# Performance work log

Measured on AMD Instinct MI355X. Metric: run time of the kernel, lower is better.

Reference implementation:

```python
import jax, jax.numpy as jnp
import numpy as np

B, T, F_IN, H, OUT = 64, 2048, 128, 256, 10
K, STRIDE, C = 5, 2, 64
TC = (T - K) // STRIDE + 1  # 1022


def setup_inputs() -> dict:
    key = jax.random.key(0)
    ks = jax.random.split(key, 10)
    u = lambda k, shape, bound: jax.random.uniform(k, shape, jnp.float32, -bound, bound)
    cb = 1.0 / np.sqrt(F_IN * K)   # torch Conv1d init bound
    lb = 1.0 / np.sqrt(H)          # torch LSTMCell / Linear init bound
    return {
        "input": jax.random.normal(ks[0], (B, T, F_IN), jnp.float32),
        "r": jnp.zeros((TC, B, C), jnp.float32),
        "conv_w": u(ks[1], (C, F_IN, K), cb),
        "conv_b": u(ks[2], (C,), cb),
        "w_ih": u(ks[3], (4 * H, C), lb),
        "w_hh": u(ks[4], (4 * H, H), lb),
        "b_ih": u(ks[5], (4 * H,), lb),
        "b_hh": u(ks[6], (4 * H,), lb),
        "lin_w": u(ks[7], (OUT, H), lb),
        "lin_b": u(ks[8], (OUT,), lb),
        "batch_size": B,
    }


def reference(input, r, conv_w, conv_b, w_ih, w_hh, b_ih, b_hh, lin_w, lin_b, batch_size):
    # F.normalize default: L2 over dim=1 (the time axis here), eps=1e-12
    norm = jnp.sqrt(jnp.sum(input * input, axis=1, keepdims=True))
    x = input / jnp.maximum(norm, 1e-12)
    # Conv1d over time: [B,T,F] -> [B,F,T] -> [B,64,Tc]
    x = jnp.transpose(x, (0, 2, 1))
    y = jax.lax.conv_general_dilated(
        x, conv_w, window_strides=(STRIDE,), padding='VALID',
        dimension_numbers=('NCH', 'OIH', 'NCH')) + conv_b[None, :, None]
    lstm_in = jax.nn.relu(jnp.transpose(y, (2, 0, 1)))  # [Tc, B, 64]

    hdim = w_hh.shape[1]
    bsz = lstm_in.shape[1]

    def step(carry, xt):
        h, c = carry
        gates = xt @ w_ih.T + h @ w_hh.T + b_ih + b_hh
        i, f, g, o = jnp.split(gates, 4, axis=-1)  # torch gate order i,f,g,o
        c = jax.nn.sigmoid(f) * c + jax.nn.sigmoid(i) * jnp.tanh(g)
        h = jax.nn.sigmoid(o) * jnp.tanh(c)
        return (h, c), None

    init = (jnp.zeros((bsz, hdim), lstm_in.dtype), jnp.zeros((bsz, hdim), lstm_in.dtype))
    (h_t, _), _ = jax.lax.scan(step, init, lstm_in)
    return h_t @ lin_w.T + lin_b
```

## Files before the change

### kernel.cpp

```cpp
#include <hip/hip_runtime.h>
#include <stdint.h>

#define B_ 64
#define T_ 2048
#define F_ 128
#define H_ 256
#define TC_ 1022

typedef __bf16 bf16x8 __attribute__((ext_vector_type(8)));
typedef float f32x4 __attribute__((ext_vector_type(4)));
typedef uint u32x4 __attribute__((ext_vector_type(4)));
typedef unsigned long long u64;

__device__ __forceinline__ ushort f2bf(float f) {
    uint32_t u = __builtin_bit_cast(uint32_t, f);
    u += 0x7FFFu + ((u >> 16) & 1u);
    return (ushort)(u >> 16);
}
__device__ __forceinline__ float sigmoidf_(float x) {
    return __builtin_amdgcn_rcpf(1.f + __expf(-x));
}
__device__ __forceinline__ float tanhf_(float x) {
    x = fminf(15.f, fmaxf(-15.f, x));
    float e = __expf(2.f * x);
    return 1.f - 2.f * __builtin_amdgcn_rcpf(e + 1.f);
}

__global__ __launch_bounds__(128) void k_sqsum(const float* __restrict__ in,
                                               float* __restrict__ sq) {
    int b = blockIdx.x >> 4, tq = blockIdx.x & 15, f = threadIdx.x;
    const float* p = in + ((size_t)b * T_ + (size_t)tq * 128) * F_ + f;
    float acc = 0.f;
#pragma unroll 8
    for (int t = 0; t < 128; ++t) { float v = p[(size_t)t * F_]; acc += v * v; }
    atomicAdd(&sq[b * F_ + f], acc);
}

__global__ __launch_bounds__(256) void k_prep(const float* __restrict__ wih, const float* __restrict__ whh,
                                              const float* __restrict__ bih, const float* __restrict__ bhh,
                                              ushort* __restrict__ wbf, float* __restrict__ bias) {
    int e = blockIdx.x * 256 + threadIdx.x;
    if (e < 64 * 16 * 320) {
        int g = e / 5120, m = (e / 320) & 15, k = e % 320;
        int j = (m & 3) * 256 + g * 4 + (m >> 2);
        float v = (k < 64) ? wih[j * 64 + k] : whh[j * 256 + (k - 64)];
        wbf[e] = f2bf(v);
    }
    if (e < 1024) bias[e] = bih[e] + bhh[e];
}

__global__ __launch_bounds__(256) void k_conv(const float* __restrict__ in, const float* __restrict__ cw,
                                              const float* __restrict__ cb, const float* __restrict__ sq,
                                              ushort* __restrict__ li) {
    __shared__ float rn[128];
    __shared__ __align__(16) float xs[67 * 129];
    __shared__ __align__(16) float wl[80 * 68];
    int b = blockIdx.x >> 5, tile = blockIdx.x & 31;
    int tc0 = tile * 32;
    int tid = threadIdx.x;
    if (tid < 128) { float ss = sq[b * 128 + tid]; rn[tid] = 1.f / fmaxf(sqrtf(ss), 1e-12f); }
    __syncthreads();
    const float* ip = in + ((size_t)b * T_ + (size_t)(2 * tc0)) * F_;
    for (int i = tid; i < 67 * 128; i += 256) {
        int r = i >> 7, f = i & 127;
        int t = 2 * tc0 + r;
        xs[r * 129 + f] = (t < T_) ? ip[(size_t)r * F_ + f] * rn[f] : 0.f;
    }
    int cg = tid & 15, tcg = tid >> 4;
    float a00 = 0, a01 = 0, a10 = 0, a11 = 0, a20 = 0, a21 = 0, a30 = 0, a31 = 0;
    for (int fc = 0; fc < 8; ++fc) {
        __syncthreads();
        for (int i = tid; i < 64 * 80; i += 256) {
            int c = i / 80, j = i - c * 80;
            wl[j * 68 + c] = cw[c * 640 + fc * 80 + j];
        }
        __syncthreads();
#pragma unroll
        for (int fi = 0; fi < 16; ++fi) {
#pragma unroll
            for (int k = 0; k < 5; ++k) {
                const float4 w4 = *(const float4*)&wl[(fi * 5 + k) * 68 + cg * 4];
                float x0 = xs[(4 * tcg + k) * 129 + fc * 16 + fi];
                float x1 = xs[(4 * tcg + 2 + k) * 129 + fc * 16 + fi];
                a00 += w4.x * x0; a01 += w4.x * x1;
                a10 += w4.y * x0; a11 += w4.y * x1;
                a20 += w4.z * x0; a21 += w4.z * x1;
                a30 += w4.w * x0; a31 += w4.w * x1;
            }
        }
    }
    float bc0 = cb[cg * 4 + 0], bc1 = cb[cg * 4 + 1], bc2 = cb[cg * 4 + 2], bc3 = cb[cg * 4 + 3];
#pragma unroll
    for (int tt = 0; tt < 2; ++tt) {
        int tc = tc0 + tcg * 2 + tt;
        if (tc < TC_) {
            float v0 = fmaxf((tt ? a01 : a00) + bc0, 0.f);
            float v1 = fmaxf((tt ? a11 : a10) + bc1, 0.f);
            float v2 = fmaxf((tt ? a21 : a20) + bc2, 0.f);
            float v3 = fmaxf((tt ? a31 : a30) + bc3, 0.f);
            uint2 pk;
            pk.x = (uint32_t)f2bf(v0) | ((uint32_t)f2bf(v1) << 16);
            pk.y = (uint32_t)f2bf(v2) | ((uint32_t)f2bf(v3) << 16);
            *reinterpret_cast<uint2*>(&li[((size_t)tc * 64 + b) * 72 + cg * 4]) = pk;
        }
    }
}

__global__ __launch_bounds__(512) void k_scan(const ushort* __restrict__ li,
                                              const ushort* __restrict__ wbf,
                                              const float* __restrict__ bias,
                                              u64* __restrict__ hbuf,
                                              float* __restrict__ hfin) {
    __shared__ __align__(16) ushort Hs[2][16 * 264];
    int p = blockIdx.x & 7, q = blockIdx.x >> 3;
    if (p >= 4) return;
    int tid = threadIdx.x;
    int lane = tid & 63, wave = tid >> 6, l16 = lane & 15, quad = lane >> 4;
    int bb = p * 16 + l16;
    int g2a = q * 16 + 2 * wave, g2b = g2a + 1;
    int u0 = g2a * 4 + quad, u1 = g2b * 4 + quad;
    int pc = 32 * q + 4 * wave + (quad >> 1);
    bf16x8 af0[10], af1[10];
    const ushort* wp0 = wbf + ((size_t)(g2a * 16 + l16)) * 320 + quad * 8;
    const ushort* wp1 = wbf + ((size_t)(g2b * 16 + l16)) * 320 + quad * 8;
#pragma unroll
    for (int s = 0; s < 10; ++s) { af0[s] = *(const bf16x8*)(wp0 + s * 32);
                                   af1[s] = *(const bf16x8*)(wp1 + s * 32); }
    float bi0 = bias[u0], bf0 = bias[256 + u0], bg0 = bias[512 + u0], bo0 = bias[768 + u0];
    float bi1 = bias[u1], bf1 = bias[256 + u1], bg1 = bias[512 + u1], bo1 = bias[768 + u1];
    float cs0 = 0.f, cs1 = 0.f;
    bool broken = false;
    const ushort* xpp = li + ((size_t)0 * 64 + bb) * 72 + quad * 8;
    bf16x8 x0 = *(const bf16x8*)xpp;
    bf16x8 x1 = *(const bf16x8*)(xpp + 32);
#pragma unroll 1
    for (int t = 0; t < TC_; ++t) {
        f32x4 A0 = {0.f, 0.f, 0.f, 0.f}, A1 = {0.f, 0.f, 0.f, 0.f};
        A0 = __builtin_amdgcn_mfma_f32_16x16x32_bf16(af0[0], x0, A0, 0, 0, 0);
        A1 = __builtin_amdgcn_mfma_f32_16x16x32_bf16(af1[0], x0, A1, 0, 0, 0);
        A0 = __builtin_amdgcn_mfma_f32_16x16x32_bf16(af0[1], x1, A0, 0, 0, 0);
        A1 = __builtin_amdgcn_mfma_f32_16x16x32_bf16(af1[1], x1, A1, 0, 0, 0);
        char* hb = (char*)Hs + (size_t)(t & 1) * (16 * 264 * 2);
        if (t > 0) {
            uint tg = (uint)(t - 1);
            const u64* src = hbuf + ((size_t)((t - 1) & 1) << 13) + p * 2048 + tid * 4;
            u64 vv0, vv1, vv2, vv3;
            bool got = false;
            if (!broken) {
                u32x4 pa, pb;
                bool ok;
                int guard = 0;
                do {
                    asm volatile(
                        "global_load_dwordx4 %0, %2, off sc0\n\t"
                        "global_load_dwordx4 %1, %2, off offset:16 sc0\n\t"
                        "s_waitcnt vmcnt(0)"
                        : "=&v"(pa), "=&v"(pb)
                        : "v"(src)
                        : "memory");
                    uint m = ((pa.x >> 16) ^ tg) | ((pa.y >> 16) ^ tg)
                           | ((pa.z >> 16) ^ tg) | ((pa.w >> 16) ^ tg)
                           | ((pb.x >> 16) ^ tg) | ((pb.y >> 16) ^ tg)
                           | ((pb.z >> 16) ^ tg) | ((pb.w >> 16) ^ tg);
                    ok = (m == 0);
                } while (!__all(ok) && ++guard < 1024);
                got = __all(ok);
                if (got) {
                    vv0 = ((u64)pa.y << 32) | pa.x;
                    vv1 = ((u64)pa.w << 32) | pa.z;
                    vv2 = ((u64)pb.y << 32) | pb.x;
                    vv3 = ((u64)pb.w << 32) | pb.z;
                } else {
                    broken = true;
                }
            }
            if (!got) {
                u64 w0, w1, w2, w3;
                bool ok;
                int guard = 0;
                do {
                    w0 = __hip_atomic_load(src + 0, __ATOMIC_RELAXED, __HIP_MEMORY_SCOPE_AGENT);
                    w1 = __hip_atomic_load(src + 1, __ATOMIC_RELAXED, __HIP_MEMORY_SCOPE_AGENT);
                    w2 = __hip_atomic_load(src + 2, __ATOMIC_RELAXED, __HIP_MEMORY_SCOPE_AGENT);
                    w3 = __hip_atomic_load(src + 3, __ATOMIC_RELAXED, __HIP_MEMORY_SCOPE_AGENT);
                    uint m = (((uint)(w0 >> 16) & 0xFFFFu) ^ tg) | (((uint)(w0 >> 48)) ^ tg);
                    m |= (((uint)(w1 >> 16) & 0xFFFFu) ^ tg) | (((uint)(w1 >> 48)) ^ tg);
                    m |= (((uint)(w2 >> 16) & 0xFFFFu) ^ tg) | (((uint)(w2 >> 48)) ^ tg);
                    m |= (((uint)(w3 >> 16) & 0xFFFFu) ^ tg) | (((uint)(w3 >> 48)) ^ tg);
                    ok = (m == 0);
                } while (!__all(ok) && ++guard < (1 << 14));
                vv0 = w0; vv1 = w1; vv2 = w2; vv3 = w3;
            }
            {
                int b = tid >> 5, c0 = (tid * 4) & 127;
                uint4 w;
                w.x = ((uint)vv0 & 0xFFFFu) | (((uint)(vv0 >> 32) & 0xFFFFu) << 16);
                w.y = ((uint)vv1 & 0xFFFFu) | (((uint)(vv1 >> 32) & 0xFFFFu) << 16);
                w.z = ((uint)vv2 & 0xFFFFu) | (((uint)(vv2 >> 32) & 0xFFFFu) << 16);
                w.w = ((uint)vv3 & 0xFFFFu) | (((uint)(vv3 >> 32) & 0xFFFFu) << 16);
                *(uint4*)(hb + b * 528 + c0 * 4) = w;
            }
            __syncthreads();
#pragma unroll
            for (int s = 0; s < 8; ++s) {
                bf16x8 bh = *(const bf16x8*)(hb + l16 * 528 + s * 64 + quad * 16);
                A0 = __builtin_amdgcn_mfma_f32_16x16x32_bf16(af0[2 + s], bh, A0, 0, 0, 0);
                A1 = __builtin_amdgcn_mfma_f32_16x16x32_bf16(af1[2 + s], bh, A1, 0, 0, 0);
            }
        }
        float hv0, hv1;
        {
            float gi = A0[0] + bi0, gf = A0[1] + bf0, gg = A0[2] + bg0, go = A0[3] + bo0;
            float ii = sigmoidf_(gi), ff = sigmoidf_(gf), g2 = tanhf_(gg), oo = sigmoidf_(go);
            cs0 = ff * cs0 + ii * g2;
            hv0 = oo * tanhf_(cs0);
        }
        {
            float gi = A1[0] + bi1, gf = A1[1] + bf1, gg = A1[2] + bg1, go = A1[3] + bo1;
            float ii = sigmoidf_(gi), ff = sigmoidf_(gf), g2 = tanhf_(gg), oo = sigmoidf_(go);
            cs1 = ff * cs1 + ii * g2;
            hv1 = oo * tanhf_(cs1);
        }
        if (t == TC_ - 1) {
            hfin[u0 * 64 + bb] = hv0;
            hfin[u1 * 64 + bb] = hv1;
        } else {
            ushort h0 = f2bf(hv0), h1 = f2bf(hv1);
            uint pr0 = ((uint)h0 & 0xFFFFu) | ((uint)__shfl((int)h0, (lane + 16) & 63) << 16);
            uint pr1 = ((uint)h1 & 0xFFFFu) | ((uint)__shfl((int)h1, (lane + 16) & 63) << 16);
            if ((quad & 1) == 0) {
                uint tg2 = ((uint)t) << 16;
                u64 w0 = (u64)((pr0 & 0xFFFFu) | tg2) | ((u64)((pr0 >> 16) | tg2) << 32);
                u64 w1 = (u64)((pr1 & 0xFFFFu) | tg2) | ((u64)((pr1 >> 16) | tg2) << 32);
                u64* dst = hbuf + ((size_t)(t & 1) << 13) + p * 2048 + l16 * 128;
                __hip_atomic_store(dst + pc, w0, __ATOMIC_RELAXED, __HIP_MEMORY_SCOPE_AGENT);
                __hip_atomic_store(dst + pc + 2, w1, __ATOMIC_RELAXED, __HIP_MEMORY_SCOPE_AGENT);
            }
        }
        int tn = (t + 1 < TC_) ? t + 1 : t;
        const ushort* xpn = li + ((size_t)tn * 64 + bb) * 72 + quad * 8;
        x0 = *(const bf16x8*)xpn;
        x1 = *(const bf16x8*)(xpn + 32);
    }
}

__global__ __launch_bounds__(64) void k_fin(const float* __restrict__ hfin, const float* __restrict__ lw,
                                            const float* __restrict__ lb, float* __restrict__ out) {
    int o = blockIdx.x, b = threadIdx.x;
    float acc = lb[o];
    const float* wp = lw + o * 256;
#pragma unroll 4
    for (int u2 = 0; u2 < 256; ++u2) acc += hfin[u2 * 64 + b] * wp[u2];
    out[b * 10 + o] = acc;
}

extern "C" void kernel_launch(void* const* d_in, const int* in_sizes, int n_in,
                              void* d_out, int out_size, void* d_ws, size_t ws_size,
                              hipStream_t stream) {
    const float* in  = (const float*)d_in[0];
    const float* cw  = (const float*)d_in[2];
    const float* cb  = (const float*)d_in[3];
    const float* wih = (const float*)d_in[4];
    const float* whh = (const float*)d_in[5];
    const float* bih = (const float*)d_in[6];
    const float* bhh = (const float*)d_in[7];
    const float* lw  = (const float*)d_in[8];
    const float* lb  = (const float*)d_in[9];
    float* out = (float*)d_out;

    char* ws = (char*)d_ws;
    float*  sq   = (float*)(ws + 0);
    u64*    hbuf = (u64*)(ws + 32768);
    float*  bias = (float*)(ws + 163840);
    float*  hfin = (float*)(ws + 167936);
    ushort* wbf  = (ushort*)(ws + 233472);
    ushort* li   = (ushort*)(ws + 888832);

    hipMemsetAsync(sq, 0, 32768, stream);
    hipMemsetAsync(hbuf, 0xFF, 131072, stream);

    k_sqsum<<<1024, 128, 0, stream>>>(in, sq);
    k_prep<<<1280, 256, 0, stream>>>(wih, whh, bih, bhh, wbf, bias);
    k_conv<<<2048, 256, 0, stream>>>(in, cw, cb, sq, li);
    k_scan<<<32, 512, 0, stream>>>(li, wbf, bias, hbuf, hfin);
    k_fin<<<10, 64, 0, stream>>>(hfin, lw, lb, out);
}
```

Baseline: 2.547 ms.

## Repartition LSTM scan into fewer, larger 1024-thread blocks

The recurrent scan kernel now runs 16 blocks of 1024 threads, so 8 blocks are active instead of 16. Each active block covers half of the hidden units rather than a quarter, so each batch group exchanges hidden state across 2 blocks instead of 4. Each thread now polls and copies half as much of the shared hidden-state buffer per step. The aim is to cut the cost of the cross-block flag polling on every timestep. In exchange, twice as many waves share each CU's matrix units and the block-wide barrier has more waves to wait for.

```diff
diff --git a/kernel.cpp b/kernel.cpp
--- a/kernel.cpp
+++ b/kernel.cpp
@@ -106,20 +106,20 @@
     }
 }
 
-__global__ __launch_bounds__(512) void k_scan(const ushort* __restrict__ li,
-                                              const ushort* __restrict__ wbf,
-                                              const float* __restrict__ bias,
-                                              u64* __restrict__ hbuf,
-                                              float* __restrict__ hfin) {
+__global__ __launch_bounds__(1024) void k_scan(const ushort* __restrict__ li,
+                                               const ushort* __restrict__ wbf,
+                                               const float* __restrict__ bias,
+                                               u64* __restrict__ hbuf,
+                                               float* __restrict__ hfin) {
     __shared__ __align__(16) ushort Hs[2][16 * 264];
     int p = blockIdx.x & 7, q = blockIdx.x >> 3;
     if (p >= 4) return;
     int tid = threadIdx.x;
     int lane = tid & 63, wave = tid >> 6, l16 = lane & 15, quad = lane >> 4;
     int bb = p * 16 + l16;
-    int g2a = q * 16 + 2 * wave, g2b = g2a + 1;
+    int g2a = q * 32 + wave * 2, g2b = g2a + 1;
     int u0 = g2a * 4 + quad, u1 = g2b * 4 + quad;
-    int pc = 32 * q + 4 * wave + (quad >> 1);
+    int pc = 2 * g2a + (quad >> 1);
     bf16x8 af0[10], af1[10];
     const ushort* wp0 = wbf + ((size_t)(g2a * 16 + l16)) * 320 + quad * 8;
     const ushort* wp1 = wbf + ((size_t)(g2b * 16 + l16)) * 320 + quad * 8;
@@ -143,62 +143,47 @@
         char* hb = (char*)Hs + (size_t)(t & 1) * (16 * 264 * 2);
         if (t > 0) {
             uint tg = (uint)(t - 1);
-            const u64* src = hbuf + ((size_t)((t - 1) & 1) << 13) + p * 2048 + tid * 4;
-            u64 vv0, vv1, vv2, vv3;
+            const u64* src = hbuf + ((size_t)((t - 1) & 1) << 13) + p * 2048 + tid * 2;
+            u64 vv0, vv1;
             bool got = false;
             if (!broken) {
-                u32x4 pa, pb;
+                u32x4 pa;
                 bool ok;
                 int guard = 0;
                 do {
                     asm volatile(
-                        "global_load_dwordx4 %0, %2, off sc0\n\t"
-                        "global_load_dwordx4 %1, %2, off offset:16 sc0\n\t"
+                        "global_load_dwordx4 %0, %1, off sc0\n\t"
                         "s_waitcnt vmcnt(0)"
-                        : "=&v"(pa), "=&v"(pb)
-                        : "v"(src)
-                        : "memory");
+                        : "=&v"(pa) : "v"(src) : "memory");
                     uint m = ((pa.x >> 16) ^ tg) | ((pa.y >> 16) ^ tg)
-                           | ((pa.z >> 16) ^ tg) | ((pa.w >> 16) ^ tg)
-                           | ((pb.x >> 16) ^ tg) | ((pb.y >> 16) ^ tg)
-                           | ((pb.z >> 16) ^ tg) | ((pb.w >> 16) ^ tg);
+                           | ((pa.z >> 16) ^ tg) | ((pa.w >> 16) ^ tg);
                     ok = (m == 0);
                 } while (!__all(ok) && ++guard < 1024);
                 got = __all(ok);
                 if (got) {
                     vv0 = ((u64)pa.y << 32) | pa.x;
                     vv1 = ((u64)pa.w << 32) | pa.z;
-                    vv2 = ((u64)pb.y << 32) | pb.x;
-                    vv3 = ((u64)pb.w << 32) | pb.z;
-                } else {
-                    broken = true;
-                }
+                } else broken = true;
             }
             if (!got) {
-                u64 w0, w1, w2, w3;
+                u64 w0, w1;
                 bool ok;
                 int guard = 0;
                 do {
                     w0 = __hip_atomic_load(src + 0, __ATOMIC_RELAXED, __HIP_MEMORY_SCOPE_AGENT);
                     w1 = __hip_atomic_load(src + 1, __ATOMIC_RELAXED, __HIP_MEMORY_SCOPE_AGENT);
-                    w2 = __hip_atomic_load(src + 2, __ATOMIC_RELAXED, __HIP_MEMORY_SCOPE_AGENT);
-                    w3 = __hip_atomic_load(src + 3, __ATOMIC_RELAXED, __HIP_MEMORY_SCOPE_AGENT);
                     uint m = (((uint)(w0 >> 16) & 0xFFFFu) ^ tg) | (((uint)(w0 >> 48)) ^ tg);
                     m |= (((uint)(w1 >> 16) & 0xFFFFu) ^ tg) | (((uint)(w1 >> 48)) ^ tg);
-                    m |= (((uint)(w2 >> 16) & 0xFFFFu) ^ tg) | (((uint)(w2 >> 48)) ^ tg);
-                    m |= (((uint)(w3 >> 16) & 0xFFFFu) ^ tg) | (((uint)(w3 >> 48)) ^ tg);
                     ok = (m == 0);
                 } while (!__all(ok) && ++guard < (1 << 14));
-                vv0 = w0; vv1 = w1; vv2 = w2; vv3 = w3;
+                vv0 = w0; vv1 = w1;
             }
             {
-                int b = tid >> 5, c0 = (tid * 4) & 127;
-                uint4 w;
+                int b = tid >> 6, c0 = (tid & 63) * 2;
+                uint2 w;
                 w.x = ((uint)vv0 & 0xFFFFu) | (((uint)(vv0 >> 32) & 0xFFFFu) << 16);
                 w.y = ((uint)vv1 & 0xFFFFu) | (((uint)(vv1 >> 32) & 0xFFFFu) << 16);
-                w.z = ((uint)vv2 & 0xFFFFu) | (((uint)(vv2 >> 32) & 0xFFFFu) << 16);
-                w.w = ((uint)vv3 & 0xFFFFu) | (((uint)(vv3 >> 32) & 0xFFFFu) << 16);
-                *(uint4*)(hb + b * 528 + c0 * 4) = w;
+                *(uint2*)(hb + b * 528 + c0 * 4) = w;
             }
             __syncthreads();
 #pragma unroll
@@ -282,6 +267,6 @@
     k_sqsum<<<1024, 128, 0, stream>>>(in, sq);
     k_prep<<<1280, 256, 0, stream>>>(wih, whh, bih, bhh, wbf, bias);
     k_conv<<<2048, 256, 0, stream>>>(in, cw, cb, sq, li);
-    k_scan<<<32, 512, 0, stream>>>(li, wbf, bias, hbuf, hfin);
+    k_scan<<<16, 1024, 0, stream>>>(li, wbf, bias, hbuf, hfin);
     k_fin<<<10, 64, 0, stream>>>(hfin, lw, lb, out);
 }
```

After: 7.308 ms. +187.0%, slower.
